# Kernel tuning notes

Measured on AMD Instinct MI355X. Metric: run time of the kernel, lower is better.

## Reference

```python
import jax, jax.numpy as jnp
import numpy as np

EPS = 1e-6
GROUPS = 32


def group_norm(x, scale, bias):
    # x: [b, c, d, h, w]
    b, c, d, h, w = x.shape
    xg = x.reshape(b, GROUPS, c // GROUPS, d, h, w)
    mean = xg.mean(axis=(2, 3, 4, 5), keepdims=True)
    var = xg.var(axis=(2, 3, 4, 5), keepdims=True)
    xn = ((xg - mean) * jax.lax.rsqrt(var + EPS)).reshape(b, c, d, h, w)
    return xn * scale[None, :, None, None, None] + bias[None, :, None, None, None]


def setup_inputs() -> dict:
    key = jax.random.key(0)
    ks = jax.random.split(key, 6)
    C = 512
    x = jax.random.normal(ks[0], (2, C, 16, 16, 16), dtype=jnp.float32)
    s = 1.0 / np.sqrt(C)
    return {
        "x": x,
        "gn_scale": jnp.ones((C,), jnp.float32),
        "gn_bias": jnp.zeros((C,), jnp.float32),
        "wq": jax.random.normal(ks[1], (C, C), jnp.float32) * s,
        "bq": jnp.zeros((C,), jnp.float32),
        "wk": jax.random.normal(ks[2], (C, C), jnp.float32) * s,
        "bk": jnp.zeros((C,), jnp.float32),
        "wv": jax.random.normal(ks[3], (C, C), jnp.float32) * s,
        "bv": jnp.zeros((C,), jnp.float32),
        "wproj": jax.random.normal(ks[4], (C, C), jnp.float32) * s,
        "bproj": jnp.zeros((C,), jnp.float32),
    }


def reference(x, gn_scale, gn_bias, wq, bq, wk, bk, wv, bv, wproj, bproj):
    b, c, d, h, w = x.shape
    h_ = group_norm(x, gn_scale, gn_bias)
    hf = h_.reshape(b, c, d * h * w)  # [b, c, N]
    # 1x1x1 convs == per-position channel matmuls
    q = jnp.einsum("oc,bcn->bon", wq, hf) + bq[None, :, None]
    k = jnp.einsum("oc,bcn->bon", wk, hf) + bk[None, :, None]
    v = jnp.einsum("oc,bcn->bon", wv, hf) + bv[None, :, None]
    # attn[b, i, j] = softmax_j(q_i . k_j / sqrt(c))
    attn = jnp.einsum("bci,bcj->bij", q, k) * (c ** -0.5)
    attn = jax.nn.softmax(attn, axis=-1)
    # out[b, c, i] = sum_j v[b, c, j] * attn[b, i, j]
    out = jnp.einsum("bcj,bij->bci", v, attn)
    out = jnp.einsum("oc,bcn->bon", wproj, out) + bproj[None, :, None]
    return x + out.reshape(b, c, d, h, w)
```

## Files before the change

kernel.cpp:

```cpp
#include <hip/hip_runtime.h>
#include <hip/hip_bf16.h>

#define BB 2
#define CC 512
#define GG 32
#define NN 4096
#define EPSV 1e-6f

typedef __attribute__((ext_vector_type(4))) float f32x4;
typedef __attribute__((ext_vector_type(8))) short s16x8;
typedef __attribute__((ext_vector_type(4))) short s16x4;

__device__ __forceinline__ ushort f2bf(float f){
  union { float f; unsigned u; } v; v.f = f;
  unsigned r = v.u + 0x7fffu + ((v.u >> 16) & 1u);
  return (ushort)(r >> 16);
}
__device__ __forceinline__ short f2bfs(float f){ return (short)f2bf(f); }
__device__ __forceinline__ float b2f(ushort u){
  union { unsigned u; float f; } v; v.u = ((unsigned)u) << 16; return v.f;
}

__device__ __forceinline__ f32x4 mfma16(s16x8 a, s16x8 b, f32x4 c){
  return __builtin_amdgcn_mfma_f32_16x16x32_bf16(a, b, c, 0, 0, 0);
}

#define GLOAD_LDS16(g, l) __builtin_amdgcn_global_load_lds( \
    (const __attribute__((address_space(1))) void*)(g),     \
    (__attribute__((address_space(3))) void*)(l), 16, 0, 0)

__global__ __launch_bounds__(256) void k_convert_w(const float* __restrict__ wq, const float* __restrict__ wk,
                                                   const float* __restrict__ wv, const float* __restrict__ wp,
                                                   ushort* __restrict__ wbf){
  int idx = blockIdx.x * 256 + threadIdx.x;
  const float* srcs[4] = {wq, wk, wv, wp};
  #pragma unroll
  for (int m = 0; m < 4; m++){
    float4 v = reinterpret_cast<const float4*>(srcs[m])[idx];
    ushort4 o; o.x = f2bf(v.x); o.y = f2bf(v.y); o.z = f2bf(v.z); o.w = f2bf(v.w);
    reinterpret_cast<ushort4*>(wbf + (size_t)m * CC * CC)[idx] = o;
  }
}

__global__ __launch_bounds__(256) void k_gn_stats(const float* __restrict__ x, float* __restrict__ stats){
  int bg = blockIdx.x;
  const float* p = x + (size_t)bg * (16 * NN);
  float s = 0.f, ss = 0.f;
  for (int i = threadIdx.x; i < 16 * NN / 4; i += 256){
    float4 v = reinterpret_cast<const float4*>(p)[i];
    s  += v.x + v.y + v.z + v.w;
    ss += v.x*v.x + v.y*v.y + v.z*v.z + v.w*v.w;
  }
  #pragma unroll
  for (int off = 32; off; off >>= 1){ s += __shfl_down(s, off); ss += __shfl_down(ss, off); }
  __shared__ float rs_[4], rss_[4];
  int w = threadIdx.x >> 6, lane = threadIdx.x & 63;
  if (lane == 0){ rs_[w] = s; rss_[w] = ss; }
  __syncthreads();
  if (threadIdx.x == 0){
    float S = rs_[0] + rs_[1] + rs_[2] + rs_[3];
    float SS = rss_[0] + rss_[1] + rss_[2] + rss_[3];
    float inv = 1.0f / (16.0f * NN);
    float mean = S * inv;
    float var = SS * inv - mean * mean;
    stats[bg * 2 + 0] = mean;
    stats[bg * 2 + 1] = rsqrtf(var + EPSV);
  }
}

__global__ __launch_bounds__(256) void k_gn_apply(const float* __restrict__ x, const float* __restrict__ gsc,
                                                  const float* __restrict__ gbi, const float* __restrict__ stats,
                                                  ushort* __restrict__ hf){
  __shared__ ushort tr[32][520];
  int b = blockIdx.y;
  int nb = blockIdx.x * 32;
  int t = threadIdx.x;
  int n = t & 31, cr = t >> 5;
  const float* xb = x + (size_t)b * CC * NN;
  for (int c0 = 0; c0 < CC; c0 += 8){
    int c = c0 + cr;
    float mean = stats[(b * GG + (c >> 4)) * 2 + 0];
    float rstd = stats[(b * GG + (c >> 4)) * 2 + 1];
    float v = xb[(size_t)c * NN + nb + n];
    tr[n][c] = f2bf((v - mean) * rstd * gsc[c] + gbi[c]);
  }
  __syncthreads();
  ushort* out = hf + ((size_t)b * NN + nb) * CC;
  int c8 = (t & 63) * 8;
  int nrow0 = t >> 6;
  #pragma unroll
  for (int i = 0; i < 8; i++){
    int nr = nrow0 + i * 4;
    *reinterpret_cast<s16x8*>(&out[(size_t)nr * CC + c8]) =
      *reinterpret_cast<const s16x8*>(&tr[nr][c8]);
  }
}

__global__ __launch_bounds__(256, 3) void k_gemm_qkv2(const ushort* __restrict__ W, const ushort* __restrict__ Bt,
                                                      const float* __restrict__ bq, const float* __restrict__ bk,
                                                      const float* __restrict__ bv,
                                                      ushort* __restrict__ qo, ushort* __restrict__ ko,
                                                      ushort* __restrict__ vo, float rs){
  __shared__ __align__(16) char smem[40960];
  __shared__ float bl[3][64];
  int b = blockIdx.z, ob = blockIdx.y * 64, nb = blockIdx.x * 128;
  int t = threadIdx.x, w = t >> 6, l = t & 63;
  int lr = l & 15, lk = l >> 4;
  int wo = (w >> 1) * 32, wn = (w & 1) * 64;
  if (t < 64){ bl[0][t] = bq[ob + t]; bl[1][t] = bk[ob + t]; bl[2][t] = bv[ob + t]; }
  const ushort* Bp = Bt + ((size_t)b * NN + nb) * CC;
  const ushort* Wp = W + (size_t)ob * CC;
  int srow = l >> 2;
  int schunk = (l & 3) ^ ((l >> 2) & 3) ^ ((l >> 4) & 3);
  int xs = (lk ^ (lr & 3) ^ ((lr >> 2) & 3)) * 8;

#define STAGE_QKV(BUF, K0)                                                               \
  {                                                                                      \
    ushort* As_ = (ushort*)(smem + (BUF) * 20480);                                       \
    ushort* Bs_ = As_ + 6144;                                                            \
    _Pragma("unroll")                                                                    \
    for (int tt = 0; tt < 5; tt++){                                                      \
      int inst = w * 5 + tt;                                                             \
      if (inst < 12){                                                                    \
        int m = inst >> 2, sub = inst & 3;                                               \
        const ushort* src = Wp + (size_t)m * CC * CC + (size_t)(sub * 16 + srow) * CC + (K0) + schunk * 8; \
        GLOAD_LDS16(src, As_ + m * 2048 + sub * 512);                                    \
      } else {                                                                           \
        int q = inst - 12;                                                               \
        const ushort* src = Bp + (size_t)(q * 16 + srow) * CC + (K0) + schunk * 8;       \
        GLOAD_LDS16(src, Bs_ + q * 512);                                                 \
      }                                                                                  \
    }                                                                                    \
  }

  f32x4 acc[3][2][4] = {};
  STAGE_QKV(0, 0)
  __syncthreads();
  for (int s16 = 0; s16 < 16; s16++){
    if (s16 < 15) STAGE_QKV((s16 + 1) & 1, (s16 + 1) * 32)
    const ushort* As = (const ushort*)(smem + (s16 & 1) * 20480);
    const ushort* Bs = As + 6144;
    s16x8 bf[4];
    #pragma unroll
    for (int sn = 0; sn < 4; sn++)
      bf[sn] = *(const s16x8*)&Bs[(wn + sn * 16 + lr) * 32 + xs];
    #pragma unroll
    for (int m = 0; m < 3; m++){
      s16x8 a0 = *(const s16x8*)&As[m * 2048 + (wo + lr) * 32 + xs];
      s16x8 a1 = *(const s16x8*)&As[m * 2048 + (wo + 16 + lr) * 32 + xs];
      #pragma unroll
      for (int sn = 0; sn < 4; sn++){
        acc[m][0][sn] = mfma16(a0, bf[sn], acc[m][0][sn]);
        acc[m][1][sn] = mfma16(a1, bf[sn], acc[m][1][sn]);
      }
    }
    __syncthreads();
  }
#undef STAGE_QKV
  #pragma unroll
  for (int m = 0; m < 2; m++){
    ushort* dst = (m == 0) ? qo : ko;
    float scl = (m == 0) ? rs : 1.0f;
    #pragma unroll
    for (int so = 0; so < 2; so++)
      #pragma unroll
      for (int sn = 0; sn < 4; sn++){
        int o0 = wo + so * 16 + lk * 4;
        int n  = nb + wn + sn * 16 + lr;
        s16x4 pv;
        #pragma unroll
        for (int r = 0; r < 4; r++) pv[r] = f2bfs((acc[m][so][sn][r] + bl[m][o0 + r]) * scl);
        *reinterpret_cast<s16x4*>(&dst[((size_t)b * NN + n) * CC + ob + o0]) = pv;
      }
  }
  ushort* Ve = (ushort*)smem;
  #pragma unroll
  for (int so = 0; so < 2; so++)
    #pragma unroll
    for (int sn = 0; sn < 4; sn++){
      int o0 = wo + so * 16 + lk * 4;
      int ncl = wn + sn * 16 + lr;
      #pragma unroll
      for (int r = 0; r < 4; r++) Ve[(o0 + r) * 136 + ncl] = f2bf(acc[2][so][sn][r] + bl[2][o0 + r]);
    }
  __syncthreads();
  {
    int row = t >> 2, cs = (t & 3) * 32;
    ushort* dst = &vo[((size_t)b * CC + ob + row) * NN + nb + cs];
    #pragma unroll
    for (int k = 0; k < 4; k++)
      *(s16x8*)&dst[k * 8] = *(const s16x8*)&Ve[row * 136 + cs + k * 8];
  }
}

__global__ __launch_bounds__(512, 2) void k_gemm_s(const ushort* __restrict__ qt, const ushort* __restrict__ kt,
                                                   ushort* __restrict__ P, float* __restrict__ part){
  extern __shared__ __align__(16) char smem[];
  int lin = blockIdx.x + 16 * blockIdx.y + 256 * blockIdx.z;
  int tt0 = (lin & 7) * 64 + (lin >> 3);
  int jblk = tt0 & 15;
  int pair = tt0 >> 4;
  int b = pair >> 4;
  int j0 = jblk * 256, i0 = (pair & 15) * 256;
  int t = threadIdx.x, w = t >> 6, l = t & 63;
  int lr = l & 15, lk = l >> 4;
  int wj2 = w >> 2, wi4 = w & 3;
  const ushort* kb = kt + ((size_t)b * NN + j0) * CC;
  const ushort* qb = qt + ((size_t)b * NN + i0) * CC;
  int srow = l >> 3;
  int schunk = (l & 7) ^ srow;

#define STAGE_S(BUF, K0)                                                          \
  {                                                                               \
    ushort* Ks_ = (ushort*)(smem + (BUF) * 32768);                                \
    ushort* Qs_ = (ushort*)(smem + 65536 + (BUF) * 32768);                        \
    _Pragma("unroll")                                                             \
    for (int tt = 0; tt < 8; tt++){                                               \
      int inst = w * 8 + tt;                                                      \
      if (inst < 32){                                                             \
        const ushort* src = kb + (size_t)(inst * 8 + srow) * CC + (K0) + schunk * 8; \
        GLOAD_LDS16(src, Ks_ + inst * 512);                                       \
      } else {                                                                    \
        int g = inst - 32;                                                        \
        const ushort* src = qb + (size_t)(g * 8 + srow) * CC + (K0) + schunk * 8; \
        GLOAD_LDS16(src, Qs_ + g * 512);                                          \
      }                                                                           \
    }                                                                             \
  }

  f32x4 acc[8][4] = {};
  STAGE_S(0, 0)
  for (int s8 = 0; s8 < 8; s8++){
    if (s8 < 7){
      STAGE_S((s8 + 1) & 1, (s8 + 1) * 64)
      asm volatile("s_waitcnt vmcnt(8)" ::: "memory");
    } else {
      asm volatile("s_waitcnt vmcnt(0)" ::: "memory");
    }
    __builtin_amdgcn_s_barrier();
    __builtin_amdgcn_sched_barrier(0);
    const ushort* Ks = (const ushort*)(smem + (s8 & 1) * 32768);
    const ushort* Qs = (const ushort*)(smem + 65536 + (s8 & 1) * 32768);
    #pragma unroll
    for (int kk = 0; kk < 2; kk++){
      int xs = ((kk * 4 + lk) ^ (lr & 7)) * 8;
      s16x8 bf[4];
      #pragma unroll
      for (int si = 0; si < 4; si++)
        bf[si] = *(const s16x8*)&Qs[(wi4 * 64 + si * 16 + lr) * 64 + xs];
      #pragma unroll
      for (int sj = 0; sj < 8; sj++){
        s16x8 a = *(const s16x8*)&Ks[(wj2 * 128 + sj * 16 + lr) * 64 + xs];
        #pragma unroll
        for (int si = 0; si < 4; si++)
          acc[sj][si] = mfma16(a, bf[si], acc[sj][si]);
      }
    }
    asm volatile("s_waitcnt lgkmcnt(0)" ::: "memory");
    __builtin_amdgcn_s_barrier();
    __builtin_amdgcn_sched_barrier(0);
  }
#undef STAGE_S
  ushort* Pe = (ushort*)smem;
  float rsum[4] = {0.f, 0.f, 0.f, 0.f};
  #pragma unroll
  for (int pass = 0; pass < 2; pass++){
    if ((wi4 >> 1) == pass){
      #pragma unroll
      for (int sj = 0; sj < 8; sj++)
        #pragma unroll
        for (int si = 0; si < 4; si++){
          int il = (wi4 & 1) * 64 + si * 16 + lr;
          int jl = wj2 * 128 + sj * 16 + lk * 4;
          s16x4 pk;
          #pragma unroll
          for (int r = 0; r < 4; r++){
            float e = __builtin_amdgcn_exp2f(acc[sj][si][r]);
            pk[r] = f2bfs(e);
            rsum[si] += e;
          }
          *(s16x4*)&Pe[il * 264 + jl] = pk;
        }
    }
    __syncthreads();
    {
      int row = t >> 2, cs = (t & 3) * 64;
      ushort* dst = P + ((size_t)b * NN + i0 + pass * 128 + row) * NN + j0 + cs;
      #pragma unroll
      for (int k = 0; k < 8; k++)
        *(s16x8*)&dst[k * 8] = *(const s16x8*)&Pe[row * 264 + cs + k * 8];
    }
    __syncthreads();
  }
  #pragma unroll
  for (int si = 0; si < 4; si++){
    float s = rsum[si];
    s += __shfl_xor(s, 16);
    s += __shfl_xor(s, 32);
    if (lk == 0){
      int il = wi4 * 64 + si * 16 + lr;
      part[((size_t)b * NN + i0 + il) * 32 + jblk * 2 + wj2] = s;
    }
  }
}

__global__ __launch_bounds__(256) void k_rowsum2(const float* __restrict__ part, float* __restrict__ linv){
  int row = blockIdx.x * 4 + (threadIdx.x >> 6);
  int l = threadIdx.x & 63;
  float s = (l < 32) ? part[(size_t)row * 32 + l] : 0.f;
  #pragma unroll
  for (int off = 32; off; off >>= 1) s += __shfl_down(s, off);
  if (l == 0) linv[row] = 1.0f / s;
}

__global__ __launch_bounds__(512) void k_gemm_o(const ushort* __restrict__ P, const ushort* __restrict__ vv,
                                                const float* __restrict__ linv, ushort* __restrict__ ot){
  __shared__ __align__(16) char smem[49152];
  int lin = blockIdx.x + 8 * blockIdx.y + 256 * blockIdx.z;
  int tt0 = (lin & 7) * 64 + (lin >> 3);
  int cblk = tt0 & 7;
  int pair = tt0 >> 3;
  int b = pair >> 5;
  int c0 = cblk * 64, i0 = (pair & 31) * 128;
  int t = threadIdx.x, w = t >> 6, l = t & 63;
  int lr = l & 15, lk = l >> 4;
  int wi = (w >> 1) * 32, wc = (w & 1) * 32;
  const ushort* vb = vv + ((size_t)b * CC + c0) * NN;
  const ushort* pb = P + ((size_t)b * NN + i0) * NN;
  int srow = l >> 3;
  int schunk = (l & 7) ^ srow;

#define STAGE_O(BUF, K0)                                                          \
  {                                                                               \
    ushort* Vs_ = (ushort*)(smem + (BUF) * 8192);                                 \
    ushort* Ps_ = (ushort*)(smem + 16384 + (BUF) * 16384);                        \
    _Pragma("unroll")                                                             \
    for (int tt = 0; tt < 3; tt++){                                               \
      int inst = w * 3 + tt;                                                      \
      if (inst < 8){                                                              \
        const ushort* src = vb + (size_t)(inst * 8 + srow) * NN + (K0) + schunk * 8; \
        GLOAD_LDS16(src, Vs_ + inst * 512);                                       \
      } else {                                                                    \
        int q = inst - 8;                                                         \
        const ushort* src = pb + (size_t)(q * 8 + srow) * NN + (K0) + schunk * 8; \
        GLOAD_LDS16(src, Ps_ + q * 512);                                          \
      }                                                                           \
    }                                                                             \
  }

  f32x4 acc[2][2] = {};
  STAGE_O(0, 0)
  for (int s64 = 0; s64 < 64; s64++){
    if (s64 < 63){
      STAGE_O((s64 + 1) & 1, (s64 + 1) * 64)
      asm volatile("s_waitcnt vmcnt(3)" ::: "memory");
    } else {
      asm volatile("s_waitcnt vmcnt(0)" ::: "memory");
    }
    __builtin_amdgcn_s_barrier();
    __builtin_amdgcn_sched_barrier(0);
    const ushort* Vs = (const ushort*)(smem + (s64 & 1) * 8192);
    const ushort* Ps = (const ushort*)(smem + 16384 + (s64 & 1) * 16384);
    #pragma unroll
    for (int kk = 0; kk < 2; kk++){
      int xs = ((kk * 4 + lk) ^ (lr & 7)) * 8;
      s16x8 af[2], bf[2];
      af[0] = *(const s16x8*)&Vs[(wc + lr) * 64 + xs];
      af[1] = *(const s16x8*)&Vs[(wc + 16 + lr) * 64 + xs];
      bf[0] = *(const s16x8*)&Ps[(wi + lr) * 64 + xs];
      bf[1] = *(const s16x8*)&Ps[(wi + 16 + lr) * 64 + xs];
      acc[0][0] = mfma16(af[0], bf[0], acc[0][0]);
      acc[0][1] = mfma16(af[0], bf[1], acc[0][1]);
      acc[1][0] = mfma16(af[1], bf[0], acc[1][0]);
      acc[1][1] = mfma16(af[1], bf[1], acc[1][1]);
    }
    asm volatile("s_waitcnt lgkmcnt(0)" ::: "memory");
    __builtin_amdgcn_s_barrier();
    __builtin_amdgcn_sched_barrier(0);
  }
#undef STAGE_O
  ushort* Oe = (ushort*)smem;
  #pragma unroll
  for (int si = 0; si < 2; si++){
    int il = wi + si * 16 + lr;
    float li = linv[(size_t)b * NN + i0 + il];
    #pragma unroll
    for (int sc = 0; sc < 2; sc++){
      int cl = wc + sc * 16 + lk * 4;
      s16x4 pk;
      #pragma unroll
      for (int r = 0; r < 4; r++) pk[r] = f2bfs(acc[sc][si][r] * li);
      *(s16x4*)&Oe[il * 72 + cl] = pk;
    }
  }
  __syncthreads();
  {
    int row = t >> 2, cs = (t & 3) * 16;
    ushort* dst = ot + ((size_t)b * NN + i0 + row) * CC + c0 + cs;
    #pragma unroll
    for (int k = 0; k < 2; k++)
      *(s16x8*)&dst[k * 8] = *(const s16x8*)&Oe[row * 72 + cs + k * 8];
  }
}

__global__ __launch_bounds__(256, 3) void k_gemm_proj2(const ushort* __restrict__ A, const ushort* __restrict__ Bt,
                                                       const float* __restrict__ bias, float* __restrict__ o32,
                                                       const float* __restrict__ xres){
  __shared__ __align__(16) char smem[34048];
  __shared__ float bl[64];
  int b = blockIdx.z, ob = blockIdx.y * 64, nb = blockIdx.x * 128;
  int t = threadIdx.x, w = t >> 6, l = t & 63;
  int lr = l & 15, lk = l >> 4;
  int wo = (w >> 1) * 32, wn = (w & 1) * 64;
  if (t < 64) bl[t] = bias[ob + t];
  const ushort* Bp = Bt + ((size_t)b * NN + nb) * CC;
  const ushort* Ap = A + (size_t)ob * CC;
  int srow = l >> 2;
  int schunk = (l & 3) ^ ((l >> 2) & 3) ^ ((l >> 4) & 3);
  int xs = (lk ^ (lr & 3) ^ ((lr >> 2) & 3)) * 8;

#define STAGE_P2(BUF, K0)                                                         \
  {                                                                               \
    ushort* As_ = (ushort*)(smem + (BUF) * 12288);                                \
    ushort* Bs_ = As_ + 2048;                                                     \
    _Pragma("unroll")                                                             \
    for (int tt = 0; tt < 3; tt++){                                               \
      int inst = w * 3 + tt;                                                      \
      if (inst < 4){                                                              \
        const ushort* src = Ap + (size_t)(inst * 16 + srow) * CC + (K0) + schunk * 8; \
        GLOAD_LDS16(src, As_ + inst * 512);                                       \
      } else {                                                                    \
        int q = inst - 4;                                                         \
        const ushort* src = Bp + (size_t)(q * 16 + srow) * CC + (K0) + schunk * 8; \
        GLOAD_LDS16(src, Bs_ + q * 512);                                          \
      }                                                                           \
    }                                                                             \
  }

  f32x4 acc[2][4] = {};
  STAGE_P2(0, 0)
  __syncthreads();
  for (int s16 = 0; s16 < 16; s16++){
    if (s16 < 15) STAGE_P2((s16 + 1) & 1, (s16 + 1) * 32)
    const ushort* As = (const ushort*)(smem + (s16 & 1) * 12288);
    const ushort* Bs = As + 2048;
    s16x8 a0 = *(const s16x8*)&As[(wo + lr) * 32 + xs];
    s16x8 a1 = *(const s16x8*)&As[(wo + 16 + lr) * 32 + xs];
    #pragma unroll
    for (int sn = 0; sn < 4; sn++){
      s16x8 bf = *(const s16x8*)&Bs[(wn + sn * 16 + lr) * 32 + xs];
      acc[0][sn] = mfma16(a0, bf, acc[0][sn]);
      acc[1][sn] = mfma16(a1, bf, acc[1][sn]);
    }
    __syncthreads();
  }
#undef STAGE_P2
  float* trf = (float*)smem;
  #pragma unroll
  for (int so = 0; so < 2; so++)
    #pragma unroll
    for (int sn = 0; sn < 4; sn++){
      int o0 = wo + so * 16 + lk * 4;
      int ncl = wn + sn * 16 + lr;
      #pragma unroll
      for (int r = 0; r < 4; r++) trf[(o0 + r) * 133 + ncl] = acc[so][sn][r] + bl[o0 + r];
    }
  __syncthreads();
  {
    int row = t >> 2, cs = (t & 3) * 32;
    size_t base = ((size_t)b * CC + ob + row) * NN + nb + cs;
    #pragma unroll
    for (int q = 0; q < 8; q++){
      float4 xv = *reinterpret_cast<const float4*>(&xres[base + q * 4]);
      float4 ov;
      ov.x = xv.x + trf[row * 133 + cs + q * 4 + 0];
      ov.y = xv.y + trf[row * 133 + cs + q * 4 + 1];
      ov.z = xv.z + trf[row * 133 + cs + q * 4 + 2];
      ov.w = xv.w + trf[row * 133 + cs + q * 4 + 3];
      *reinterpret_cast<float4*>(&o32[base + q * 4]) = ov;
    }
  }
}

extern "C" void kernel_launch(void* const* d_in, const int* in_sizes, int n_in,
                              void* d_out, int out_size, void* d_ws, size_t ws_size,
                              hipStream_t stream){
  const float* x   = (const float*)d_in[0];
  const float* gsc = (const float*)d_in[1];
  const float* gbi = (const float*)d_in[2];
  const float* wq  = (const float*)d_in[3];
  const float* bq  = (const float*)d_in[4];
  const float* wk  = (const float*)d_in[5];
  const float* bk  = (const float*)d_in[6];
  const float* wv  = (const float*)d_in[7];
  const float* bv  = (const float*)d_in[8];
  const float* wp  = (const float*)d_in[9];
  const float* bp  = (const float*)d_in[10];
  char* ws = (char*)d_ws;
  const size_t MB = 1024 * 1024;
  ushort* wbf  = (ushort*)ws;
  ushort* qtb  = (ushort*)(ws + 2 * MB);
  ushort* ktb  = (ushort*)(ws + 10 * MB);
  ushort* vvb  = (ushort*)(ws + 18 * MB);
  ushort* hfb  = (ushort*)(ws + 26 * MB);
  ushort* Pbuf = (ushort*)(ws + 34 * MB);
  float* linv  = (float*)(ws + 98 * MB);
  float* stats = (float*)(ws + 98 * MB + 64 * 1024);
  float* part  = (float*)(ws + 26 * MB);
  ushort* otb = hfb;

  const float rs = 0.044194173824159216f * 1.4426950408889634f;

  k_convert_w<<<256, 256, 0, stream>>>(wq, wk, wv, wp, wbf);
  k_gn_stats<<<64, 256, 0, stream>>>(x, stats);
  k_gn_apply<<<dim3(128, 2, 1), 256, 0, stream>>>(x, gsc, gbi, stats, hfb);
  k_gemm_qkv2<<<dim3(32, 8, 2), 256, 0, stream>>>(wbf, hfb, bq, bk, bv, qtb, ktb, vvb, rs);
  k_gemm_s<<<dim3(16, 16, 2), 512, 131072, stream>>>(qtb, ktb, Pbuf, part);
  k_rowsum2<<<2048, 256, 0, stream>>>(part, linv);
  k_gemm_o<<<dim3(8, 32, 2), 512, 0, stream>>>(Pbuf, vvb, linv, otb);
  k_gemm_proj2<<<dim3(32, 8, 2), 256, 0, stream>>>(wbf + 3 * CC * CC, otb, bp, (float*)d_out, x);
}
```

Measured before the change: 189.1 us.

## Widen P·V output tile to 128 channels and split GroupNorm stats reduction

The P·V GEMM now computes a 128-row by 128-channel tile per block instead of 128x64. Each wave holds 2x4 MFMA accumulators, so every P row loaded from global memory serves twice as many channels and total P traffic is halved. This needs 64KB of LDS per block and launches half as many blocks, which may lower occupancy. Separately, GroupNorm statistics are split into a 256-block partial-sum pass plus a small finalize kernel to give the reduction more parallelism, at the cost of one extra launch.

```diff
diff --git a/kernel.cpp b/kernel.cpp
--- a/kernel.cpp
+++ b/kernel.cpp
@@ -42,11 +42,11 @@
   }
 }
 
-__global__ __launch_bounds__(256) void k_gn_stats(const float* __restrict__ x, float* __restrict__ stats){
-  int bg = blockIdx.x;
-  const float* p = x + (size_t)bg * (16 * NN);
+__global__ __launch_bounds__(256) void k_gn_stats1(const float* __restrict__ x, float* __restrict__ pstat){
+  int blk = blockIdx.x;
+  const float* p = x + (size_t)blk * 16384;
   float s = 0.f, ss = 0.f;
-  for (int i = threadIdx.x; i < 16 * NN / 4; i += 256){
+  for (int i = threadIdx.x; i < 4096; i += 256){
     float4 v = reinterpret_cast<const float4*>(p)[i];
     s  += v.x + v.y + v.z + v.w;
     ss += v.x*v.x + v.y*v.y + v.z*v.z + v.w*v.w;
@@ -58,11 +58,21 @@
   if (lane == 0){ rs_[w] = s; rss_[w] = ss; }
   __syncthreads();
   if (threadIdx.x == 0){
-    float S = rs_[0] + rs_[1] + rs_[2] + rs_[3];
-    float SS = rss_[0] + rss_[1] + rss_[2] + rss_[3];
+    pstat[blk * 2 + 0] = rs_[0] + rs_[1] + rs_[2] + rs_[3];
+    pstat[blk * 2 + 1] = rss_[0] + rss_[1] + rss_[2] + rss_[3];
+  }
+}
+__global__ __launch_bounds__(64) void k_gn_stats2(const float* __restrict__ pstat, float* __restrict__ stats){
+  int bg = blockIdx.x;
+  int l = threadIdx.x;
+  float s = 0.f, ss = 0.f;
+  if (l < 4){ s = pstat[(bg * 4 + l) * 2]; ss = pstat[(bg * 4 + l) * 2 + 1]; }
+  #pragma unroll
+  for (int off = 2; off; off >>= 1){ s += __shfl_down(s, off); ss += __shfl_down(ss, off); }
+  if (l == 0){
     float inv = 1.0f / (16.0f * NN);
-    float mean = S * inv;
-    float var = SS * inv - mean * mean;
+    float mean = s * inv;
+    float var = ss * inv - mean * mean;
     stats[bg * 2 + 0] = mean;
     stats[bg * 2 + 1] = rsqrtf(var + EPSV);
   }
@@ -315,16 +325,16 @@
 
 __global__ __launch_bounds__(512) void k_gemm_o(const ushort* __restrict__ P, const ushort* __restrict__ vv,
                                                 const float* __restrict__ linv, ushort* __restrict__ ot){
-  __shared__ __align__(16) char smem[49152];
-  int lin = blockIdx.x + 8 * blockIdx.y + 256 * blockIdx.z;
-  int tt0 = (lin & 7) * 64 + (lin >> 3);
-  int cblk = tt0 & 7;
-  int pair = tt0 >> 3;
-  int b = pair >> 5;
-  int c0 = cblk * 64, i0 = (pair & 31) * 128;
+  __shared__ __align__(16) char smem[65536];
+  int lin = blockIdx.x + 4 * blockIdx.y + 128 * blockIdx.z;
+  int tt0 = (lin & 7) * 32 + (lin >> 3);
+  int cblk = tt0 & 3;
+  int ib   = tt0 >> 2;
+  int b = ib >> 5;
+  int c0 = cblk * 128, i0 = (ib & 31) * 128;
   int t = threadIdx.x, w = t >> 6, l = t & 63;
   int lr = l & 15, lk = l >> 4;
-  int wi = (w >> 1) * 32, wc = (w & 1) * 32;
+  int wi2 = w >> 2, wc4 = w & 3;
   const ushort* vb = vv + ((size_t)b * CC + c0) * NN;
   const ushort* pb = P + ((size_t)b * NN + i0) * NN;
   int srow = l >> 3;
@@ -332,47 +342,50 @@
 
 #define STAGE_O(BUF, K0)                                                          \
   {                                                                               \
-    ushort* Vs_ = (ushort*)(smem + (BUF) * 8192);                                 \
-    ushort* Ps_ = (ushort*)(smem + 16384 + (BUF) * 16384);                        \
+    ushort* Vs_ = (ushort*)(smem + (BUF) * 16384);                                \
+    ushort* Ps_ = (ushort*)(smem + 32768 + (BUF) * 16384);                        \
     _Pragma("unroll")                                                             \
-    for (int tt = 0; tt < 3; tt++){                                               \
-      int inst = w * 3 + tt;                                                      \
-      if (inst < 8){                                                              \
+    for (int tt = 0; tt < 4; tt++){                                               \
+      int inst = w * 4 + tt;                                                      \
+      if (inst < 16){                                                             \
         const ushort* src = vb + (size_t)(inst * 8 + srow) * NN + (K0) + schunk * 8; \
         GLOAD_LDS16(src, Vs_ + inst * 512);                                       \
       } else {                                                                    \
-        int q = inst - 8;                                                         \
-        const ushort* src = pb + (size_t)(q * 8 + srow) * NN + (K0) + schunk * 8; \
-        GLOAD_LDS16(src, Ps_ + q * 512);                                          \
+        int g = inst - 16;                                                        \
+        const ushort* src = pb + (size_t)(g * 8 + srow) * NN + (K0) + schunk * 8; \
+        GLOAD_LDS16(src, Ps_ + g * 512);                                          \
       }                                                                           \
     }                                                                             \
   }
 
-  f32x4 acc[2][2] = {};
+  f32x4 acc[2][4] = {};
   STAGE_O(0, 0)
   for (int s64 = 0; s64 < 64; s64++){
     if (s64 < 63){
       STAGE_O((s64 + 1) & 1, (s64 + 1) * 64)
-      asm volatile("s_waitcnt vmcnt(3)" ::: "memory");
+      asm volatile("s_waitcnt vmcnt(4)" ::: "memory");
     } else {
       asm volatile("s_waitcnt vmcnt(0)" ::: "memory");
     }
     __builtin_amdgcn_s_barrier();
     __builtin_amdgcn_sched_barrier(0);
-    const ushort* Vs = (const ushort*)(smem + (s64 & 1) * 8192);
-    const ushort* Ps = (const ushort*)(smem + 16384 + (s64 & 1) * 16384);
+    const ushort* Vs = (const ushort*)(smem + (s64 & 1) * 16384);
+    const ushort* Ps = (const ushort*)(smem + 32768 + (s64 & 1) * 16384);
     #pragma unroll
     for (int kk = 0; kk < 2; kk++){
       int xs = ((kk * 4 + lk) ^ (lr & 7)) * 8;
-      s16x8 af[2], bf[2];
-      af[0] = *(const s16x8*)&Vs[(wc + lr) * 64 + xs];
-      af[1] = *(const s16x8*)&Vs[(wc + 16 + lr) * 64 + xs];
-      bf[0] = *(const s16x8*)&Ps[(wi + lr) * 64 + xs];
-      bf[1] = *(const s16x8*)&Ps[(wi + 16 + lr) * 64 + xs];
-      acc[0][0] = mfma16(af[0], bf[0], acc[0][0]);
-      acc[0][1] = mfma16(af[0], bf[1], acc[0][1]);
-      acc[1][0] = mfma16(af[1], bf[0], acc[1][0]);
-      acc[1][1] = mfma16(af[1], bf[1], acc[1][1]);
+      s16x8 af[2], bf[4];
+      #pragma unroll
+      for (int sc = 0; sc < 2; sc++)
+        af[sc] = *(const s16x8*)&Vs[(wc4 * 32 + sc * 16 + lr) * 64 + xs];
+      #pragma unroll
+      for (int si = 0; si < 4; si++)
+        bf[si] = *(const s16x8*)&Ps[(wi2 * 64 + si * 16 + lr) * 64 + xs];
+      #pragma unroll
+      for (int sc = 0; sc < 2; sc++)
+        #pragma unroll
+        for (int si = 0; si < 4; si++)
+          acc[sc][si] = mfma16(af[sc], bf[si], acc[sc][si]);
     }
     asm volatile("s_waitcnt lgkmcnt(0)" ::: "memory");
     __builtin_amdgcn_s_barrier();
@@ -381,25 +394,25 @@
 #undef STAGE_O
   ushort* Oe = (ushort*)smem;
   #pragma unroll
-  for (int si = 0; si < 2; si++){
-    int il = wi + si * 16 + lr;
+  for (int si = 0; si < 4; si++){
+    int il = wi2 * 64 + si * 16 + lr;
     float li = linv[(size_t)b * NN + i0 + il];
     #pragma unroll
     for (int sc = 0; sc < 2; sc++){
-      int cl = wc + sc * 16 + lk * 4;
+      int cl = wc4 * 32 + sc * 16 + lk * 4;
       s16x4 pk;
       #pragma unroll
       for (int r = 0; r < 4; r++) pk[r] = f2bfs(acc[sc][si][r] * li);
-      *(s16x4*)&Oe[il * 72 + cl] = pk;
+      *(s16x4*)&Oe[il * 136 + cl] = pk;
     }
   }
   __syncthreads();
   {
-    int row = t >> 2, cs = (t & 3) * 16;
+    int row = t >> 2, cs = (t & 3) * 32;
     ushort* dst = ot + ((size_t)b * NN + i0 + row) * CC + c0 + cs;
     #pragma unroll
-    for (int k = 0; k < 2; k++)
-      *(s16x8*)&dst[k * 8] = *(const s16x8*)&Oe[row * 72 + cs + k * 8];
+    for (int k = 0; k < 4; k++)
+      *(s16x8*)&dst[k * 8] = *(const s16x8*)&Oe[row * 136 + cs + k * 8];
   }
 }
 
@@ -506,17 +519,19 @@
   ushort* Pbuf = (ushort*)(ws + 34 * MB);
   float* linv  = (float*)(ws + 98 * MB);
   float* stats = (float*)(ws + 98 * MB + 64 * 1024);
+  float* pstat = (float*)(ws + 98 * MB + 96 * 1024);
   float* part  = (float*)(ws + 26 * MB);
   ushort* otb = hfb;
 
   const float rs = 0.044194173824159216f * 1.4426950408889634f;
 
   k_convert_w<<<256, 256, 0, stream>>>(wq, wk, wv, wp, wbf);
-  k_gn_stats<<<64, 256, 0, stream>>>(x, stats);
+  k_gn_stats1<<<256, 256, 0, stream>>>(x, pstat);
+  k_gn_stats2<<<64, 64, 0, stream>>>(pstat, stats);
   k_gn_apply<<<dim3(128, 2, 1), 256, 0, stream>>>(x, gsc, gbi, stats, hfb);
   k_gemm_qkv2<<<dim3(32, 8, 2), 256, 0, stream>>>(wbf, hfb, bq, bk, bv, qtb, ktb, vvb, rs);
   k_gemm_s<<<dim3(16, 16, 2), 512, 131072, stream>>>(qtb, ktb, Pbuf, part);
   k_rowsum2<<<2048, 256, 0, stream>>>(part, linv);
-  k_gemm_o<<<dim3(8, 32, 2), 512, 0, stream>>>(Pbuf, vvb, linv, otb);
+  k_gemm_o<<<dim3(4, 32, 2), 512, 0, stream>>>(Pbuf, vvb, linv, otb);
   k_gemm_proj2<<<dim3(32, 8, 2), 256, 0, stream>>>(wbf + 3 * CC * CC, otb, bp, (float*)d_out, x);
 }
```

New measurement: 177.5 us. 1.07x faster.
